# Optimization experiments

Measured on AMD Instinct MI355X. Metric: run time of the kernel, lower is better.

The kernel has to match this reference:

```python
import jax, jax.numpy as jnp
import numpy as np

B = 65536
DIMS = [784, 12, 10, 8, 6, 4, 10]  # fc1..fc6 in/out dims


def setup_inputs() -> dict:
    key = jax.random.key(0)
    ks = jax.random.split(key, 1 + 2 * 6)
    inp = {"x": jax.random.normal(ks[0], (B, DIMS[0]), dtype=jnp.float32)}
    for i in range(6):
        fan_in = DIMS[i]
        bound = 1.0 / np.sqrt(fan_in)  # torch nn.Linear default init range
        inp[f"W{i+1}"] = jax.random.uniform(ks[1 + 2 * i], (fan_in, DIMS[i + 1]), jnp.float32, -bound, bound)
        inp[f"b{i+1}"] = jax.random.uniform(ks[2 + 2 * i], (DIMS[i + 1],), jnp.float32, -bound, bound)
    return inp


def reference(x, W1, b1, W2, b2, W3, b3, W4, b4, W5, b5, W6, b6):
    x = x.reshape(x.shape[0], -1)
    h1 = jnp.tanh(x @ W1 + b1)   # [B, 12]
    h2 = jnp.tanh(h1 @ W2 + b2)  # [B, 10]
    h3 = jnp.tanh(h2 @ W3 + b3)  # [B, 8]
    h4 = jnp.tanh(h3 @ W4 + b4)  # [B, 6]
    h5 = jnp.tanh(h4 @ W5 + b5)  # [B, 4]
    out = h5 @ W6 + b6           # [B, 10] logits
    return (out, h1, h2, h3, h4, h5)
```

## Files before the change

### kernel.cpp

```cpp
#include <hip/hip_runtime.h>


__device__ __forceinline__ float ftanh(float v) {
    float e = __expf(2.0f * v);
    return 1.0f - 2.0f / (e + 1.0f);
}

__global__ __launch_bounds__(256, 4)
void mlp_fused2(const float* __restrict__ x,
                const float* __restrict__ W1, const float* __restrict__ b1,
                const float* __restrict__ W2, const float* __restrict__ b2,
                const float* __restrict__ W3, const float* __restrict__ b3,
                const float* __restrict__ W4, const float* __restrict__ b4,
                const float* __restrict__ W5, const float* __restrict__ b5,
                const float* __restrict__ W6, const float* __restrict__ b6,
                float* __restrict__ out)
{
    __shared__ float4 ldsW1[2352];

    const int tid = threadIdx.x;

    const float4* w1v = (const float4*)W1;
    for (int t = tid; t < 2352; t += 256) ldsW1[t] = w1v[t];
    __syncthreads();

    const int lane = tid & 63;
    const int wave = tid >> 6;
    const int r    = lane >> 2;
    const int sub  = lane & 3;
    const int row  = (blockIdx.x << 6) + (wave << 4) + r;

    float acc[12];
#pragma unroll
    for (int j = 0; j < 12; ++j) acc[j] = 0.f;

    const float4* xrow = (const float4*)(x + (size_t)row * 784);

    for (int i = 0; i < 49; ++i) {
        float4 xv = xrow[i * 4 + sub];
        const float4* wb = ldsW1 + i * 48 + sub * 12;
#pragma unroll
        for (int dk = 0; dk < 4; ++dk) {
            float xx = (dk == 0) ? xv.x : (dk == 1) ? xv.y : (dk == 2) ? xv.z : xv.w;
            float4 w0 = wb[dk * 3 + 0];
            float4 w1 = wb[dk * 3 + 1];
            float4 w2 = wb[dk * 3 + 2];
            acc[0] += xx * w0.x;  acc[1] += xx * w0.y;  acc[2]  += xx * w0.z;  acc[3]  += xx * w0.w;
            acc[4] += xx * w1.x;  acc[5] += xx * w1.y;  acc[6]  += xx * w1.z;  acc[7]  += xx * w1.w;
            acc[8] += xx * w2.x;  acc[9] += xx * w2.y;  acc[10] += xx * w2.z;  acc[11] += xx * w2.w;
        }
    }

    float h1[12];
#pragma unroll
    for (int j = 0; j < 12; ++j) {
        float z = acc[j];
        z += __shfl_xor(z, 1);
        z += __shfl_xor(z, 2);
        h1[j] = ftanh(z + b1[j]);
    }

    float h2[10];
#pragma unroll
    for (int m = 0; m < 10; ++m) {
        float s = b2[m];
#pragma unroll
        for (int j = 0; j < 12; ++j) s += h1[j] * W2[j * 10 + m];
        h2[m] = ftanh(s);
    }

    float h3[8];
#pragma unroll
    for (int m = 0; m < 8; ++m) {
        float s = b3[m];
#pragma unroll
        for (int j = 0; j < 10; ++j) s += h2[j] * W3[j * 8 + m];
        h3[m] = ftanh(s);
    }

    float h4[6];
#pragma unroll
    for (int m = 0; m < 6; ++m) {
        float s = b4[m];
#pragma unroll
        for (int j = 0; j < 8; ++j) s += h3[j] * W4[j * 6 + m];
        h4[m] = ftanh(s);
    }

    float h5[4];
#pragma unroll
    for (int m = 0; m < 4; ++m) {
        float s = b5[m];
#pragma unroll
        for (int j = 0; j < 6; ++j) s += h4[j] * W5[j * 4 + m];
        h5[m] = ftanh(s);
    }

    float o[10];
#pragma unroll
    for (int m = 0; m < 10; ++m) {
        float s = b6[m];
#pragma unroll
        for (int j = 0; j < 4; ++j) s += h5[j] * W6[j * 10 + m];
        o[m] = s;
    }

    const size_t H1 = 655360, H2 = 1441792, H3 = 2097152, H4 = 2621440, H5 = 3014656;
    float2* po  = (float2*)(out +      (size_t)row * 10);
    float4* ph1 = (float4*)(out + H1 + (size_t)row * 12);
    float2* ph2 = (float2*)(out + H2 + (size_t)row * 10);
    float4* ph3 = (float4*)(out + H3 + (size_t)row * 8);
    float2* ph4 = (float2*)(out + H4 + (size_t)row * 6);
    float4* ph5 = (float4*)(out + H5 + (size_t)row * 4);

    if (sub == 0) {
        po[0]  = make_float2(o[0], o[1]);
        po[4]  = make_float2(o[8], o[9]);
        ph2[0] = make_float2(h2[0], h2[1]);
        ph2[4] = make_float2(h2[8], h2[9]);
        ph4[1] = make_float2(h4[2], h4[3]);
    } else if (sub == 1) {
        po[1]  = make_float2(o[2], o[3]);
        ph1[0] = make_float4(h1[0], h1[1], h1[2], h1[3]);
        ph2[1] = make_float2(h2[2], h2[3]);
        ph3[0] = make_float4(h3[0], h3[1], h3[2], h3[3]);
        ph4[2] = make_float2(h4[4], h4[5]);
    } else if (sub == 2) {
        po[2]  = make_float2(o[4], o[5]);
        ph1[1] = make_float4(h1[4], h1[5], h1[6], h1[7]);
        ph2[2] = make_float2(h2[4], h2[5]);
        ph3[1] = make_float4(h3[4], h3[5], h3[6], h3[7]);
        ph5[0] = make_float4(h5[0], h5[1], h5[2], h5[3]);
    } else {
        po[3]  = make_float2(o[6], o[7]);
        ph1[2] = make_float4(h1[8], h1[9], h1[10], h1[11]);
        ph2[3] = make_float2(h2[6], h2[7]);
        ph4[0] = make_float2(h4[0], h4[1]);
    }
}

extern "C" void kernel_launch(void* const* d_in, const int* in_sizes, int n_in,
                              void* d_out, int out_size, void* d_ws, size_t ws_size,
                              hipStream_t stream) {
    (void)in_sizes; (void)n_in; (void)d_ws; (void)ws_size; (void)out_size;
    mlp_fused2<<<1024, 256, 0, stream>>>(
        (const float*)d_in[0],
        (const float*)d_in[1],  (const float*)d_in[2],
        (const float*)d_in[3],  (const float*)d_in[4],
        (const float*)d_in[5],  (const float*)d_in[6],
        (const float*)d_in[7],  (const float*)d_in[8],
        (const float*)d_in[9],  (const float*)d_in[10],
        (const float*)d_in[11], (const float*)d_in[12],
        (float*)d_out);
}
```

Baseline: 46.53 us.

## Use bf16 dot2 for layer one with whole-wave row splitting and DPP reductions

```diff
diff --git a/kernel.cpp b/kernel.cpp
--- a/kernel.cpp
+++ b/kernel.cpp
@@ -6,136 +6,217 @@
     return 1.0f - 2.0f / (e + 1.0f);
 }
 
+__device__ __forceinline__ uint32_t cvtpk(float lo, float hi) {
+    uint32_t d;
+    asm("v_cvt_pk_bf16_f32 %0, %1, %2" : "=v"(d) : "v"(lo), "v"(hi));
+    return d;
+}
+
+__device__ __forceinline__ float dot2(uint32_t a, uint32_t b, float c) {
+    float d;
+    asm("v_dot2_f32_bf16 %0, %1, %2, %3" : "=v"(d) : "v"(a), "v"(b), "v"(c));
+    return d;
+}
+
+template <int CTRL>
+__device__ __forceinline__ float dpp_add(float v) {
+    int m = __builtin_amdgcn_update_dpp(0, __float_as_int(v), CTRL, 0xF, 0xF, false);
+    return v + __int_as_float(m);
+}
+
+__device__ __forceinline__ float rowsum16(float v) {
+    v = dpp_add<0x128>(v);
+    v = dpp_add<0x124>(v);
+    v = dpp_add<0x122>(v);
+    v = dpp_add<0x121>(v);
+    return v;
+}
+
 __global__ __launch_bounds__(256, 4)
-void mlp_fused2(const float* __restrict__ x,
-                const float* __restrict__ W1, const float* __restrict__ b1,
-                const float* __restrict__ W2, const float* __restrict__ b2,
-                const float* __restrict__ W3, const float* __restrict__ b3,
-                const float* __restrict__ W4, const float* __restrict__ b4,
-                const float* __restrict__ W5, const float* __restrict__ b5,
-                const float* __restrict__ W6, const float* __restrict__ b6,
-                float* __restrict__ out)
+void mlp_fused11(const float* __restrict__ x,
+                 const float* __restrict__ W1, const float* __restrict__ b1,
+                 const float* __restrict__ W2, const float* __restrict__ b2,
+                 const float* __restrict__ W3, const float* __restrict__ b3,
+                 const float* __restrict__ W4, const float* __restrict__ b4,
+                 const float* __restrict__ W5, const float* __restrict__ b5,
+                 const float* __restrict__ W6, const float* __restrict__ b6,
+                 float* __restrict__ out)
 {
-    __shared__ float4 ldsW1[2352];
+    __shared__ uint32_t ldsW[392 * 13];
+    __shared__ float h1p[4][8][4][12];
 
     const int tid = threadIdx.x;
 
-    const float4* w1v = (const float4*)W1;
-    for (int t = tid; t < 2352; t += 256) ldsW1[t] = w1v[t];
+    for (int t = tid; t < 4704; t += 256) {
+        int p = t / 12, j = t - p * 12;
+        ldsW[p * 13 + j] = cvtpk(W1[p * 24 + j], W1[p * 24 + 12 + j]);
+    }
     __syncthreads();
 
-    const int lane = tid & 63;
     const int wave = tid >> 6;
-    const int r    = lane >> 2;
-    const int sub  = lane & 3;
-    const int row  = (blockIdx.x << 6) + (wave << 4) + r;
-
-    float acc[12];
-#pragma unroll
-    for (int j = 0; j < 12; ++j) acc[j] = 0.f;
-
-    const float4* xrow = (const float4*)(x + (size_t)row * 784);
-
-    for (int i = 0; i < 49; ++i) {
-        float4 xv = xrow[i * 4 + sub];
-        const float4* wb = ldsW1 + i * 48 + sub * 12;
-#pragma unroll
-        for (int dk = 0; dk < 4; ++dk) {
-            float xx = (dk == 0) ? xv.x : (dk == 1) ? xv.y : (dk == 2) ? xv.z : xv.w;
-            float4 w0 = wb[dk * 3 + 0];
-            float4 w1 = wb[dk * 3 + 1];
-            float4 w2 = wb[dk * 3 + 2];
-            acc[0] += xx * w0.x;  acc[1] += xx * w0.y;  acc[2]  += xx * w0.z;  acc[3]  += xx * w0.w;
-            acc[4] += xx * w1.x;  acc[5] += xx * w1.y;  acc[6]  += xx * w1.z;  acc[7]  += xx * w1.w;
-            acc[8] += xx * w2.x;  acc[9] += xx * w2.y;  acc[10] += xx * w2.z;  acc[11] += xx * w2.w;
+    const int L    = tid & 63;
+    const int row0 = (blockIdx.x << 5) + (wave << 3);
+    const float* xr = x + (size_t)row0 * 784;
+
+    const int  tp   = 384 + (L & 7);
+    const bool tact = (L < 8);
+
+    for (int pass = 0; pass < 4; ++pass) {
+        const float* pA = xr + (size_t)(2 * pass) * 784;
+        const float* pB = pA + 784;
+
+        float accA[12], accB[12];
+#pragma unroll
+        for (int j = 0; j < 12; ++j) { accA[j] = 0.f; accB[j] = 0.f; }
+
+#pragma unroll
+        for (int s = 0; s < 3; ++s) {
+            float4 xa = *(const float4*)(pA + 4 * (s * 64 + L));
+            float4 xb = *(const float4*)(pB + 4 * (s * 64 + L));
+            const int p0 = 2 * (s * 64 + L);
+
+            uint32_t w0[12], w1[12];
+#pragma unroll
+            for (int j = 0; j < 12; ++j) {
+                w0[j] = ldsW[p0 * 13 + j];
+                w1[j] = ldsW[p0 * 13 + 13 + j];
+            }
+
+            uint32_t xa0 = cvtpk(xa.x, xa.y), xa1 = cvtpk(xa.z, xa.w);
+            uint32_t xb0 = cvtpk(xb.x, xb.y), xb1 = cvtpk(xb.z, xb.w);
+
+#pragma unroll
+            for (int j = 0; j < 12; ++j) {
+                accA[j] = dot2(xa0, w0[j], accA[j]);
+                accA[j] = dot2(xa1, w1[j], accA[j]);
+                accB[j] = dot2(xb0, w0[j], accB[j]);
+                accB[j] = dot2(xb1, w1[j], accB[j]);
+            }
+        }
+        {
+            float2 ta = *(const float2*)(pA + 2 * tp);
+            float2 tb = *(const float2*)(pB + 2 * tp);
+            uint32_t xpa = tact ? cvtpk(ta.x, ta.y) : 0u;
+            uint32_t xpb = tact ? cvtpk(tb.x, tb.y) : 0u;
+            uint32_t wt[12];
+#pragma unroll
+            for (int j = 0; j < 12; ++j) wt[j] = ldsW[tp * 13 + j];
+#pragma unroll
+            for (int j = 0; j < 12; ++j) {
+                accA[j] = dot2(xpa, wt[j], accA[j]);
+                accB[j] = dot2(xpb, wt[j], accB[j]);
+            }
+        }
+
+#pragma unroll
+        for (int j = 0; j < 12; ++j) {
+            accA[j] = rowsum16(accA[j]);
+            accB[j] = rowsum16(accB[j]);
+        }
+        if ((L & 15) == 0) {
+            const int g = L >> 4;
+            float4* qa = (float4*)&h1p[wave][2 * pass][g][0];
+            qa[0] = make_float4(accA[0], accA[1], accA[2],  accA[3]);
+            qa[1] = make_float4(accA[4], accA[5], accA[6],  accA[7]);
+            qa[2] = make_float4(accA[8], accA[9], accA[10], accA[11]);
+            float4* qb = (float4*)&h1p[wave][2 * pass + 1][g][0];
+            qb[0] = make_float4(accB[0], accB[1], accB[2],  accB[3]);
+            qb[1] = make_float4(accB[4], accB[5], accB[6],  accB[7]);
+            qb[2] = make_float4(accB[8], accB[9], accB[10], accB[11]);
         }
     }
 
-    float h1[12];
-#pragma unroll
-    for (int j = 0; j < 12; ++j) {
-        float z = acc[j];
-        z += __shfl_xor(z, 1);
-        z += __shfl_xor(z, 2);
-        h1[j] = ftanh(z + b1[j]);
-    }
-
-    float h2[10];
-#pragma unroll
-    for (int m = 0; m < 10; ++m) {
-        float s = b2[m];
-#pragma unroll
-        for (int j = 0; j < 12; ++j) s += h1[j] * W2[j * 10 + m];
-        h2[m] = ftanh(s);
-    }
-
-    float h3[8];
-#pragma unroll
-    for (int m = 0; m < 8; ++m) {
-        float s = b3[m];
-#pragma unroll
-        for (int j = 0; j < 10; ++j) s += h2[j] * W3[j * 8 + m];
-        h3[m] = ftanh(s);
-    }
-
-    float h4[6];
-#pragma unroll
-    for (int m = 0; m < 6; ++m) {
-        float s = b4[m];
-#pragma unroll
-        for (int j = 0; j < 8; ++j) s += h3[j] * W4[j * 6 + m];
-        h4[m] = ftanh(s);
-    }
-
-    float h5[4];
-#pragma unroll
-    for (int m = 0; m < 4; ++m) {
-        float s = b5[m];
-#pragma unroll
-        for (int j = 0; j < 6; ++j) s += h4[j] * W5[j * 4 + m];
-        h5[m] = ftanh(s);
-    }
-
-    float o[10];
-#pragma unroll
-    for (int m = 0; m < 10; ++m) {
-        float s = b6[m];
-#pragma unroll
-        for (int j = 0; j < 4; ++j) s += h5[j] * W6[j * 10 + m];
-        o[m] = s;
-    }
-
-    const size_t H1 = 655360, H2 = 1441792, H3 = 2097152, H4 = 2621440, H5 = 3014656;
-    float2* po  = (float2*)(out +      (size_t)row * 10);
-    float4* ph1 = (float4*)(out + H1 + (size_t)row * 12);
-    float2* ph2 = (float2*)(out + H2 + (size_t)row * 10);
-    float4* ph3 = (float4*)(out + H3 + (size_t)row * 8);
-    float2* ph4 = (float2*)(out + H4 + (size_t)row * 6);
-    float4* ph5 = (float4*)(out + H5 + (size_t)row * 4);
-
-    if (sub == 0) {
-        po[0]  = make_float2(o[0], o[1]);
-        po[4]  = make_float2(o[8], o[9]);
-        ph2[0] = make_float2(h2[0], h2[1]);
-        ph2[4] = make_float2(h2[8], h2[9]);
-        ph4[1] = make_float2(h4[2], h4[3]);
-    } else if (sub == 1) {
-        po[1]  = make_float2(o[2], o[3]);
-        ph1[0] = make_float4(h1[0], h1[1], h1[2], h1[3]);
-        ph2[1] = make_float2(h2[2], h2[3]);
-        ph3[0] = make_float4(h3[0], h3[1], h3[2], h3[3]);
-        ph4[2] = make_float2(h4[4], h4[5]);
-    } else if (sub == 2) {
-        po[2]  = make_float2(o[4], o[5]);
-        ph1[1] = make_float4(h1[4], h1[5], h1[6], h1[7]);
-        ph2[2] = make_float2(h2[4], h2[5]);
-        ph3[1] = make_float4(h3[4], h3[5], h3[6], h3[7]);
-        ph5[0] = make_float4(h5[0], h5[1], h5[2], h5[3]);
-    } else {
-        po[3]  = make_float2(o[6], o[7]);
-        ph1[2] = make_float4(h1[8], h1[9], h1[10], h1[11]);
-        ph2[3] = make_float2(h2[6], h2[7]);
-        ph4[0] = make_float2(h4[0], h4[1]);
+    if (L < 32) {
+        const int r   = L >> 2;
+        const int sub = L & 3;
+        const int row = row0 + r;
+
+        const float4* pp = (const float4*)&h1p[wave][r][sub][0];
+        float4 a0 = pp[0], a1 = pp[1], a2 = pp[2];
+
+        float h1[12];
+#define REDJ(dst, v0)                                                      \
+        { float v = (v0); v += __shfl_xor(v, 1); v += __shfl_xor(v, 2); dst = v; }
+        REDJ(h1[0],  a0.x) REDJ(h1[1],  a0.y) REDJ(h1[2],  a0.z) REDJ(h1[3],  a0.w)
+        REDJ(h1[4],  a1.x) REDJ(h1[5],  a1.y) REDJ(h1[6],  a1.z) REDJ(h1[7],  a1.w)
+        REDJ(h1[8],  a2.x) REDJ(h1[9],  a2.y) REDJ(h1[10], a2.z) REDJ(h1[11], a2.w)
+#undef REDJ
+#pragma unroll
+        for (int j = 0; j < 12; ++j) h1[j] = ftanh(h1[j] + b1[j]);
+
+        float h2[10];
+#pragma unroll
+        for (int m = 0; m < 10; ++m) {
+            float s = b2[m];
+#pragma unroll
+            for (int j = 0; j < 12; ++j) s += h1[j] * W2[j * 10 + m];
+            h2[m] = ftanh(s);
+        }
+        float h3[8];
+#pragma unroll
+        for (int m = 0; m < 8; ++m) {
+            float s = b3[m];
+#pragma unroll
+            for (int j = 0; j < 10; ++j) s += h2[j] * W3[j * 8 + m];
+            h3[m] = ftanh(s);
+        }
+        float h4[6];
+#pragma unroll
+        for (int m = 0; m < 6; ++m) {
+            float s = b4[m];
+#pragma unroll
+            for (int j = 0; j < 8; ++j) s += h3[j] * W4[j * 6 + m];
+            h4[m] = ftanh(s);
+        }
+        float h5[4];
+#pragma unroll
+        for (int m = 0; m < 4; ++m) {
+            float s = b5[m];
+#pragma unroll
+            for (int j = 0; j < 6; ++j) s += h4[j] * W5[j * 4 + m];
+            h5[m] = ftanh(s);
+        }
+        float o[10];
+#pragma unroll
+        for (int m = 0; m < 10; ++m) {
+            float s = b6[m];
+#pragma unroll
+            for (int j = 0; j < 4; ++j) s += h5[j] * W6[j * 10 + m];
+            o[m] = s;
+        }
+
+        const size_t H1 = 655360, H2 = 1441792, H3 = 2097152, H4 = 2621440, H5 = 3014656;
+        float2* po  = (float2*)(out +      (size_t)row * 10);
+        float4* ph1 = (float4*)(out + H1 + (size_t)row * 12);
+        float2* ph2 = (float2*)(out + H2 + (size_t)row * 10);
+        float4* ph3 = (float4*)(out + H3 + (size_t)row * 8);
+        float2* ph4 = (float2*)(out + H4 + (size_t)row * 6);
+        float4* ph5 = (float4*)(out + H5 + (size_t)row * 4);
+
+        if (sub == 0) {
+            po[0]  = make_float2(o[0], o[1]);
+            po[4]  = make_float2(o[8], o[9]);
+            ph2[0] = make_float2(h2[0], h2[1]);
+            ph2[4] = make_float2(h2[8], h2[9]);
+            ph4[1] = make_float2(h4[2], h4[3]);
+        } else if (sub == 1) {
+            po[1]  = make_float2(o[2], o[3]);
+            ph1[0] = make_float4(h1[0], h1[1], h1[2], h1[3]);
+            ph2[1] = make_float2(h2[2], h2[3]);
+            ph3[0] = make_float4(h3[0], h3[1], h3[2], h3[3]);
+            ph4[2] = make_float2(h4[4], h4[5]);
+        } else if (sub == 2) {
+            po[2]  = make_float2(o[4], o[5]);
+            ph1[1] = make_float4(h1[4], h1[5], h1[6], h1[7]);
+            ph2[2] = make_float2(h2[4], h2[5]);
+            ph3[1] = make_float4(h3[4], h3[5], h3[6], h3[7]);
+            ph5[0] = make_float4(h5[0], h5[1], h5[2], h5[3]);
+        } else {
+            po[3]  = make_float2(o[6], o[7]);
+            ph1[2] = make_float4(h1[8], h1[9], h1[10], h1[11]);
+            ph2[3] = make_float2(h2[6], h2[7]);
+            ph4[0] = make_float2(h4[0], h4[1]);
+        }
     }
 }
 
@@ -143,7 +224,7 @@
                               void* d_out, int out_size, void* d_ws, size_t ws_size,
                               hipStream_t stream) {
     (void)in_sizes; (void)n_in; (void)d_ws; (void)ws_size; (void)out_size;
-    mlp_fused2<<<1024, 256, 0, stream>>>(
+    mlp_fused11<<<2048, 256, 0, stream>>>(
         (const float*)d_in[0],
         (const float*)d_in[1],  (const float*)d_in[2],
         (const float*)d_in[3],  (const float*)d_in[4],
```

Result: slower. 64.65 us (+38.9%).

## Stage x tile transposed as bf16 in LDS and split K across waves

Applied to the files above, without the earlier changes.

```diff
diff --git a/kernel.cpp b/kernel.cpp
--- a/kernel.cpp
+++ b/kernel.cpp
@@ -6,136 +6,181 @@
     return 1.0f - 2.0f / (e + 1.0f);
 }
 
-__global__ __launch_bounds__(256, 4)
-void mlp_fused2(const float* __restrict__ x,
-                const float* __restrict__ W1, const float* __restrict__ b1,
-                const float* __restrict__ W2, const float* __restrict__ b2,
-                const float* __restrict__ W3, const float* __restrict__ b3,
-                const float* __restrict__ W4, const float* __restrict__ b4,
-                const float* __restrict__ W5, const float* __restrict__ b5,
-                const float* __restrict__ W6, const float* __restrict__ b6,
-                float* __restrict__ out)
+__device__ __forceinline__ uint32_t cvtpk(float lo, float hi) {
+    uint32_t d;
+    asm("v_cvt_pk_bf16_f32 %0, %1, %2" : "=v"(d) : "v"(lo), "v"(hi));
+    return d;
+}
+
+__global__ __launch_bounds__(512, 4)
+void mlp_fused13(const float* __restrict__ x,
+                 const float* __restrict__ W1, const float* __restrict__ b1,
+                 const float* __restrict__ W2, const float* __restrict__ b2,
+                 const float* __restrict__ W3, const float* __restrict__ b3,
+                 const float* __restrict__ W4, const float* __restrict__ b4,
+                 const float* __restrict__ W5, const float* __restrict__ b5,
+                 const float* __restrict__ W6, const float* __restrict__ b6,
+                 float* __restrict__ out)
 {
-    __shared__ float4 ldsW1[2352];
-
-    const int tid = threadIdx.x;
-
-    const float4* w1v = (const float4*)W1;
-    for (int t = tid; t < 2352; t += 256) ldsW1[t] = w1v[t];
+    __shared__ uint32_t xT[392 * 33];
+    __shared__ float    pt[32 * 97];
+
+    const int tid  = threadIdx.x;
+    const int wave = tid >> 6;
+    const int lane = tid & 63;
+    const size_t row0 = (size_t)blockIdx.x << 5;
+
+#pragma unroll
+    for (int i = 0; i < 4; ++i) {
+        const int r = 8 * i + wave;
+        const float* xp = x + (row0 + r) * 784;
+#pragma unroll
+        for (int j = 0; j < 3; ++j) {
+            float4 v = *(const float4*)(xp + 256 * j + 4 * lane);
+            uint32_t q0 = cvtpk(v.x, v.y);
+            uint32_t q1 = cvtpk(v.z, v.w);
+            const int p0 = 128 * j + 2 * lane;
+            xT[p0 * 33 + r]       = q0;
+            xT[(p0 + 1) * 33 + r] = q1;
+        }
+        if (lane < 4) {
+            float4 v = *(const float4*)(xp + 768 + 4 * lane);
+            uint32_t q0 = cvtpk(v.x, v.y);
+            uint32_t q1 = cvtpk(v.z, v.w);
+            const int p0 = 384 + 2 * lane;
+            xT[p0 * 33 + r]       = q0;
+            xT[(p0 + 1) * 33 + r] = q1;
+        }
+    }
     __syncthreads();
 
-    const int lane = tid & 63;
-    const int wave = tid >> 6;
-    const int r    = lane >> 2;
-    const int sub  = lane & 3;
-    const int row  = (blockIdx.x << 6) + (wave << 4) + r;
-
-    float acc[12];
-#pragma unroll
-    for (int j = 0; j < 12; ++j) acc[j] = 0.f;
-
-    const float4* xrow = (const float4*)(x + (size_t)row * 784);
-
-    for (int i = 0; i < 49; ++i) {
-        float4 xv = xrow[i * 4 + sub];
-        const float4* wb = ldsW1 + i * 48 + sub * 12;
-#pragma unroll
-        for (int dk = 0; dk < 4; ++dk) {
-            float xx = (dk == 0) ? xv.x : (dk == 1) ? xv.y : (dk == 2) ? xv.z : xv.w;
-            float4 w0 = wb[dk * 3 + 0];
-            float4 w1 = wb[dk * 3 + 1];
-            float4 w2 = wb[dk * 3 + 2];
-            acc[0] += xx * w0.x;  acc[1] += xx * w0.y;  acc[2]  += xx * w0.z;  acc[3]  += xx * w0.w;
-            acc[4] += xx * w1.x;  acc[5] += xx * w1.y;  acc[6]  += xx * w1.z;  acc[7]  += xx * w1.w;
-            acc[8] += xx * w2.x;  acc[9] += xx * w2.y;  acc[10] += xx * w2.z;  acc[11] += xx * w2.w;
+    {
+        const int r = lane & 31;
+        float acc[12];
+#pragma unroll
+        for (int j = 0; j < 12; ++j) acc[j] = 0.f;
+
+        const int pbase = 49 * wave;
+#pragma unroll 7
+        for (int t = 0; t < 49; ++t) {
+            const int p = pbase + t;
+            uint32_t ux = xT[p * 33 + r];
+            float xlo = __uint_as_float(ux << 16);
+            float xhi = __uint_as_float(ux & 0xffff0000u);
+            const float* wk = W1 + (size_t)p * 24;
+#pragma unroll
+            for (int j = 0; j < 12; ++j) acc[j] += xlo * wk[j];
+#pragma unroll
+            for (int j = 0; j < 12; ++j) acc[j] += xhi * wk[12 + j];
+        }
+        if (lane < 32) {
+#pragma unroll
+            for (int j = 0; j < 12; ++j) pt[r * 97 + wave * 12 + j] = acc[j];
         }
     }
-
-    float h1[12];
-#pragma unroll
-    for (int j = 0; j < 12; ++j) {
-        float z = acc[j];
-        z += __shfl_xor(z, 1);
-        z += __shfl_xor(z, 2);
-        h1[j] = ftanh(z + b1[j]);
-    }
-
-    float h2[10];
-#pragma unroll
-    for (int m = 0; m < 10; ++m) {
-        float s = b2[m];
-#pragma unroll
-        for (int j = 0; j < 12; ++j) s += h1[j] * W2[j * 10 + m];
-        h2[m] = ftanh(s);
-    }
-
-    float h3[8];
-#pragma unroll
-    for (int m = 0; m < 8; ++m) {
-        float s = b3[m];
-#pragma unroll
-        for (int j = 0; j < 10; ++j) s += h2[j] * W3[j * 8 + m];
-        h3[m] = ftanh(s);
-    }
-
-    float h4[6];
-#pragma unroll
-    for (int m = 0; m < 6; ++m) {
-        float s = b4[m];
-#pragma unroll
-        for (int j = 0; j < 8; ++j) s += h3[j] * W4[j * 6 + m];
-        h4[m] = ftanh(s);
-    }
-
-    float h5[4];
-#pragma unroll
-    for (int m = 0; m < 4; ++m) {
-        float s = b5[m];
-#pragma unroll
-        for (int j = 0; j < 6; ++j) s += h4[j] * W5[j * 4 + m];
-        h5[m] = ftanh(s);
-    }
-
-    float o[10];
-#pragma unroll
-    for (int m = 0; m < 10; ++m) {
-        float s = b6[m];
-#pragma unroll
-        for (int j = 0; j < 4; ++j) s += h5[j] * W6[j * 10 + m];
-        o[m] = s;
-    }
-
-    const size_t H1 = 655360, H2 = 1441792, H3 = 2097152, H4 = 2621440, H5 = 3014656;
-    float2* po  = (float2*)(out +      (size_t)row * 10);
-    float4* ph1 = (float4*)(out + H1 + (size_t)row * 12);
-    float2* ph2 = (float2*)(out + H2 + (size_t)row * 10);
-    float4* ph3 = (float4*)(out + H3 + (size_t)row * 8);
-    float2* ph4 = (float2*)(out + H4 + (size_t)row * 6);
-    float4* ph5 = (float4*)(out + H5 + (size_t)row * 4);
-
-    if (sub == 0) {
-        po[0]  = make_float2(o[0], o[1]);
-        po[4]  = make_float2(o[8], o[9]);
-        ph2[0] = make_float2(h2[0], h2[1]);
-        ph2[4] = make_float2(h2[8], h2[9]);
-        ph4[1] = make_float2(h4[2], h4[3]);
-    } else if (sub == 1) {
-        po[1]  = make_float2(o[2], o[3]);
-        ph1[0] = make_float4(h1[0], h1[1], h1[2], h1[3]);
-        ph2[1] = make_float2(h2[2], h2[3]);
-        ph3[0] = make_float4(h3[0], h3[1], h3[2], h3[3]);
-        ph4[2] = make_float2(h4[4], h4[5]);
-    } else if (sub == 2) {
-        po[2]  = make_float2(o[4], o[5]);
-        ph1[1] = make_float4(h1[4], h1[5], h1[6], h1[7]);
-        ph2[2] = make_float2(h2[4], h2[5]);
-        ph3[1] = make_float4(h3[4], h3[5], h3[6], h3[7]);
-        ph5[0] = make_float4(h5[0], h5[1], h5[2], h5[3]);
-    } else {
-        po[3]  = make_float2(o[6], o[7]);
-        ph1[2] = make_float4(h1[8], h1[9], h1[10], h1[11]);
-        ph2[3] = make_float2(h2[6], h2[7]);
-        ph4[0] = make_float2(h4[0], h4[1]);
+    __syncthreads();
+
+    if (tid < 256) {
+        const int r  = tid >> 3;
+        const int s8 = tid & 7;
+        const int row = (int)row0 + r;
+
+        float h1[12];
+#pragma unroll
+        for (int j = 0; j < 12; ++j) {
+            float z = pt[r * 97 + s8 * 12 + j];
+            z += __shfl_xor(z, 1);
+            z += __shfl_xor(z, 2);
+            z += __shfl_xor(z, 4);
+            h1[j] = ftanh(z + b1[j]);
+        }
+
+        float h2[10];
+#pragma unroll
+        for (int m = 0; m < 10; ++m) {
+            float s = b2[m];
+#pragma unroll
+            for (int j = 0; j < 12; ++j) s += h1[j] * W2[j * 10 + m];
+            h2[m] = ftanh(s);
+        }
+        float h3[8];
+#pragma unroll
+        for (int m = 0; m < 8; ++m) {
+            float s = b3[m];
+#pragma unroll
+            for (int j = 0; j < 10; ++j) s += h2[j] * W3[j * 8 + m];
+            h3[m] = ftanh(s);
+        }
+        float h4[6];
+#pragma unroll
+        for (int m = 0; m < 6; ++m) {
+            float s = b4[m];
+#pragma unroll
+            for (int j = 0; j < 8; ++j) s += h3[j] * W4[j * 6 + m];
+            h4[m] = ftanh(s);
+        }
+        float h5[4];
+#pragma unroll
+        for (int m = 0; m < 4; ++m) {
+            float s = b5[m];
+#pragma unroll
+            for (int j = 0; j < 6; ++j) s += h4[j] * W5[j * 4 + m];
+            h5[m] = ftanh(s);
+        }
+        float o[10];
+#pragma unroll
+        for (int m = 0; m < 10; ++m) {
+            float s = b6[m];
+#pragma unroll
+            for (int j = 0; j < 4; ++j) s += h5[j] * W6[j * 10 + m];
+            o[m] = s;
+        }
+
+        const size_t H1o = 655360, H2o = 1441792, H3o = 2097152, H4o = 2621440, H5o = 3014656;
+        float2* po  = (float2*)(out +       (size_t)row * 10);
+        float4* ph1 = (float4*)(out + H1o + (size_t)row * 12);
+        float2* ph2 = (float2*)(out + H2o + (size_t)row * 10);
+        float4* ph3 = (float4*)(out + H3o + (size_t)row * 8);
+        float2* ph4 = (float2*)(out + H4o + (size_t)row * 6);
+        float4* ph5 = (float4*)(out + H5o + (size_t)row * 4);
+
+        switch (s8) {
+            case 0:
+                po[0] = make_float2(o[0], o[1]);
+                po[1] = make_float2(o[2], o[3]);
+                po[2] = make_float2(o[4], o[5]);
+                break;
+            case 1:
+                po[3] = make_float2(o[6], o[7]);
+                po[4] = make_float2(o[8], o[9]);
+                ph4[0] = make_float2(h4[0], h4[1]);
+                break;
+            case 2:
+                ph1[0] = make_float4(h1[0], h1[1], h1[2], h1[3]);
+                ph1[1] = make_float4(h1[4], h1[5], h1[6], h1[7]);
+                ph4[1] = make_float2(h4[2], h4[3]);
+                break;
+            case 3:
+                ph1[2] = make_float4(h1[8], h1[9], h1[10], h1[11]);
+                ph2[0] = make_float2(h2[0], h2[1]);
+                ph4[2] = make_float2(h4[4], h4[5]);
+                break;
+            case 4:
+                ph2[1] = make_float2(h2[2], h2[3]);
+                ph2[2] = make_float2(h2[4], h2[5]);
+                break;
+            case 5:
+                ph2[3] = make_float2(h2[6], h2[7]);
+                ph2[4] = make_float2(h2[8], h2[9]);
+                break;
+            case 6:
+                ph3[0] = make_float4(h3[0], h3[1], h3[2], h3[3]);
+                ph5[0] = make_float4(h5[0], h5[1], h5[2], h5[3]);
+                break;
+            default:
+                ph3[1] = make_float4(h3[4], h3[5], h3[6], h3[7]);
+                break;
+        }
     }
 }
 
@@ -143,7 +188,7 @@
                               void* d_out, int out_size, void* d_ws, size_t ws_size,
                               hipStream_t stream) {
     (void)in_sizes; (void)n_in; (void)d_ws; (void)ws_size; (void)out_size;
-    mlp_fused2<<<1024, 256, 0, stream>>>(
+    mlp_fused13<<<2048, 512, 0, stream>>>(
         (const float*)d_in[0],
         (const float*)d_in[1],  (const float*)d_in[2],
         (const float*)d_in[3],  (const float*)d_in[4],
```

Result: slower. 178.4 us (+283.3%).
